# Kernel tuning notes

Hardware: AMD Instinct MI355X
Metric: run time of the kernel (lower is better)

## Reference

```python
import jax, jax.numpy as jnp
import numpy as np

DIM = 180      # channel dim C
HEADS = 6      # num_heads
WS = 8         # window_size
HIDDEN = int(DIM * 4.0)  # mlp hidden = 720
HEAD_DIM = DIM // HEADS  # 30


def layernorm(x, scale, bias, eps=1e-5):
    m = jnp.mean(x, axis=-1, keepdims=True)
    v = jnp.var(x, axis=-1, keepdims=True)
    return (x - m) * jax.lax.rsqrt(v + eps) * scale + bias


def setup_inputs() -> dict:
    key = jax.random.key(0)
    ks = jax.random.split(key, 16)
    B, H, W = 4, 256, 256
    s = 0.02  # weight init scale for numerical sanity
    return {
        "x": jax.random.normal(ks[0], (B, H * W, DIM), jnp.float32),
        "norm1_scale": jnp.ones((DIM,), jnp.float32),
        "norm1_bias": jnp.zeros((DIM,), jnp.float32),
        "qkv_w": jax.random.normal(ks[1], (DIM, 3 * DIM), jnp.float32) * s,  # [in,out] == torch W.T
        "qkv_b": jax.random.normal(ks[2], (3 * DIM,), jnp.float32) * s,
        "proj_w": jax.random.normal(ks[3], (DIM, DIM), jnp.float32) * s,
        "proj_b": jax.random.normal(ks[4], (DIM,), jnp.float32) * s,
        "norm2_scale": jnp.ones((DIM,), jnp.float32),
        "norm2_bias": jnp.zeros((DIM,), jnp.float32),
        "mlp_w1": jax.random.normal(ks[5], (DIM, HIDDEN), jnp.float32) * s,
        "mlp_b1": jax.random.normal(ks[6], (HIDDEN,), jnp.float32) * s,
        "mlp_w2": jax.random.normal(ks[7], (HIDDEN, DIM), jnp.float32) * s,
        "mlp_b2": jax.random.normal(ks[8], (DIM,), jnp.float32) * s,
        "H": H,
        "W": W,
    }


def reference(x, norm1_scale, norm1_bias, qkv_w, qkv_b, proj_w, proj_b,
              norm2_scale, norm2_bias, mlp_w1, mlp_b1, mlp_w2, mlp_b2, H, W):
    B, L, C = x.shape
    shortcut = x
    h = layernorm(x, norm1_scale, norm1_bias).reshape(B, H, W, C)
    # pad to multiples of window size (no-op when H,W % WS == 0)
    pad_b = (WS - H % WS) % WS
    pad_r = (WS - W % WS) % WS
    h = jnp.pad(h, ((0, 0), (0, pad_b), (0, pad_r), (0, 0)))
    Hp, Wp = H + pad_b, W + pad_r
    # window_partition: (B,Hp,Wp,C) -> (nW*B, WS*WS, C)
    win = h.reshape(B, Hp // WS, WS, Wp // WS, WS, C)
    win = win.transpose(0, 1, 3, 2, 4, 5).reshape(-1, WS * WS, C)
    Bw, N, _ = win.shape
    # fused qkv projection
    qkv = (win @ qkv_w + qkv_b).reshape(Bw, N, 3, HEADS, HEAD_DIM)
    qkv = qkv.transpose(2, 0, 3, 1, 4)  # (3, Bw, heads, N, head_dim)
    q, k, v = qkv[0], qkv[1], qkv[2]
    q = q * (HEAD_DIM ** -0.5)
    attn = jax.nn.softmax(jnp.einsum('bhnd,bhmd->bhnm', q, k), axis=-1)
    o = jnp.einsum('bhnm,bhmd->bhnd', attn, v)
    o = o.transpose(0, 2, 1, 3).reshape(Bw, N, C)
    o = o @ proj_w + proj_b
    # window_reverse: (nW*B, WS*WS, C) -> (B,Hp,Wp,C)
    h = o.reshape(B, Hp // WS, Wp // WS, WS, WS, C)
    h = h.transpose(0, 1, 3, 2, 4, 5).reshape(B, Hp, Wp, C)
    h = h[:, :H, :W, :].reshape(B, H * W, C)
    x = shortcut + h
    # MLP with exact (erf) GELU, matching torch nn.GELU default
    y = layernorm(x, norm2_scale, norm2_bias)
    y = jax.nn.gelu(y @ mlp_w1 + mlp_b1, approximate=False) @ mlp_w2 + mlp_b2
    return x + y
```

## Files before the change

kernel.cpp:

```cpp
#include <hip/hip_runtime.h>

typedef unsigned int u32;
typedef unsigned short u16;
typedef __attribute__((ext_vector_type(8))) __bf16 bf16x8;
typedef __attribute__((ext_vector_type(4))) float f32x4;

#define MFMA(a,b,c) __builtin_amdgcn_mfma_f32_16x16x32_bf16(a,b,c,0,0,0)

__device__ __forceinline__ float bf2f(u16 v){ return __uint_as_float(((u32)v) << 16); }
__device__ __forceinline__ u16 f2bf(float f){
  u32 u = __float_as_uint(f);
  u += 0x7fffu + ((u >> 16) & 1u);
  return (u16)(u >> 16);
}
__device__ __forceinline__ u32 pack2(float a, float b){
  return (u32)f2bf(a) | ((u32)f2bf(b) << 16);
}
__device__ __forceinline__ float gelu_fast(float v){
  float t = v*(-1.5957691216f - 0.0713548163f*v*v);
  return v * __builtin_amdgcn_rcpf(1.f + __expf(t));
}

#define QSCALE 0.18257418583505536f

#define OQKV 0
#define OWP  147456
#define OW1  196608
#define OW2  344064
#define NW_TOT 532480

__global__ void swin_unpack(const float* __restrict__ qkvw, const float* __restrict__ projw,
                            const float* __restrict__ w1, const float* __restrict__ w2,
                            u16* __restrict__ ws){
  int idx = blockIdx.x * 256 + threadIdx.x;
  if (idx >= NW_TOT) return;
  float val = 0.f;
  if (idx < OWP){
    int t = idx, nt = t / 3072, r = t % 3072, kt = r >> 9, e = r & 511;
    int lane = e >> 3, j = e & 7;
    int n = nt*16 + (lane & 15), k = kt*32 + (lane >> 4)*8 + j;
    if (n < 576){
      int p = n / 192, c = n - p*192;
      if (c < 180 && k < 180){
        val = qkvw[k*540 + p*180 + c];
        if (p == 0) val *= QSCALE;
      }
    }
  } else if (idx < OW1){
    int t = idx - OWP, nt = t / 3072, r = t % 3072, kt = r >> 9, e = r & 511;
    int lane = e >> 3, j = e & 7;
    int n = nt*16 + (lane & 15), k = kt*32 + (lane >> 4)*8 + j;
    if (n < 180 && k < 180) val = projw[k*180 + n];
  } else if (idx < OW2){
    int t = idx - OW1, nt = t / 3072, r = t % 3072, kt = r >> 9, e = r & 511;
    int lane = e >> 3, j = e & 7;
    int n = nt*16 + (lane & 15), k = kt*32 + (lane >> 4)*8 + j;
    if (n < 720 && k < 180) val = w1[k*720 + n];
  } else {
    int t = idx - OW2, nt = t / 11776, r = t % 11776, kt = r >> 9, e = r & 511;
    int lane = e >> 3, j = e & 7;
    int n = nt*16 + (lane & 15), k = kt*32 + (lane >> 4)*8 + j;
    if (n < 180 && k < 720) val = w2[k*180 + n];
  }
  ws[idx] = f2bf(val);
}

#define A_Y   0
#define A_Q   25600
#define A_K   51200
#define A_VT  76800
#define A_P   104448
#define A_RB  141312

__global__ __launch_bounds__(1024, 1) void swin_attn(
    const float* __restrict__ x, const float* __restrict__ n1s, const float* __restrict__ n1b,
    const u16* __restrict__ ws, const float* __restrict__ qkvb,
    const float* __restrict__ projb, float* __restrict__ out){
  __shared__ __align__(16) char sm[141568];
  const int tid = threadIdx.x;
  const int w16 = tid >> 6, l = tid & 63, l15 = l & 15, lq = l >> 4;
  int* rb = (int*)(sm + A_RB);
  const f32x4 fz = {0.f, 0.f, 0.f, 0.f};
  float4 xv[3];
  const int r4 = l & 3, lq4 = l >> 2;
  const int myrow = w16*4 + r4;

  if (tid < 64){
    int wb = blockIdx.x;
    int b = wb >> 10, wy = (wb >> 5) & 31, wx = wb & 31;
    rb[tid] = b*65536 + (wy*8 + (tid>>3))*256 + (wx*8 + (tid&7));
  }
  for (int i = tid; i < 2304; i += 1024){
    int row = i / 36, t = i - row*36;
    if (t < 24){
      int buf = (t >= 12) ? A_K : A_Q; int tt = t % 12;
      *(u16*)(sm + buf + row*400 + ((tt>>1)*32 + 30 + (tt&1))*2) = 0;
    } else
      *(u16*)(sm + A_Y + row*400 + (180 + t - 24)*2) = 0;
  }
  __syncthreads();

  {
    const float4* px = (const float4*)(x + (size_t)rb[myrow]*180);
    xv[0] = px[lq4];
    xv[1] = px[lq4 + 16];
    xv[2] = (lq4 < 13) ? px[lq4 + 32] : make_float4(0.f,0.f,0.f,0.f);
    float s = 0.f, ss = 0.f;
    #pragma unroll
    for (int i = 0; i < 3; ++i){
      s  += xv[i].x + xv[i].y + xv[i].z + xv[i].w;
      ss += xv[i].x*xv[i].x + xv[i].y*xv[i].y + xv[i].z*xv[i].z + xv[i].w*xv[i].w;
    }
    #pragma unroll
    for (int m = 4; m <= 32; m <<= 1){ s += __shfl_xor(s, m); ss += __shfl_xor(ss, m); }
    float mean = s * (1.f/180.f);
    float rstd = rsqrtf(ss * (1.f/180.f) - mean*mean + 1e-5f);
    u32* yr = (u32*)(sm + A_Y + myrow*400);
    const float4* s4 = (const float4*)n1s;
    const float4* b4 = (const float4*)n1b;
    #pragma unroll
    for (int i = 0; i < 3; ++i){
      if (i < 2 || lq4 < 13){
        int c4 = lq4 + 16*i;
        float4 sc = s4[c4], bi = b4[c4];
        float e0 = (xv[i].x - mean)*rstd*sc.x + bi.x;
        float e1 = (xv[i].y - mean)*rstd*sc.y + bi.y;
        float e2 = (xv[i].z - mean)*rstd*sc.z + bi.z;
        float e3 = (xv[i].w - mean)*rstd*sc.w + bi.w;
        yr[c4*2]     = pack2(e0, e1);
        yr[c4*2 + 1] = pack2(e2, e3);
      }
    }
  }
  __syncthreads();

  {
    const int ntb = w16*3;
    f32x4 acc[4][3];
    #pragma unroll
    for (int m = 0; m < 4; ++m)
      #pragma unroll
      for (int i = 0; i < 3; ++i) acc[m][i] = fz;
    bf16x8 bcur[3];
    #pragma unroll
    for (int i = 0; i < 3; ++i)
      bcur[i] = *(const bf16x8*)(ws + OQKV + ((ntb+i)*6 + 0)*512 + l*8);
    #pragma unroll
    for (int kt = 0; kt < 6; ++kt){
      bf16x8 bnxt[3];
      if (kt < 5){
        #pragma unroll
        for (int i = 0; i < 3; ++i)
          bnxt[i] = *(const bf16x8*)(ws + OQKV + ((ntb+i)*6 + kt + 1)*512 + l*8);
      }
      bf16x8 a[4];
      #pragma unroll
      for (int m = 0; m < 4; ++m)
        a[m] = *(const bf16x8*)(sm + A_Y + (m*16 + l15)*400 + kt*64 + lq*16);
      #pragma unroll
      for (int m = 0; m < 4; ++m)
        #pragma unroll
        for (int i = 0; i < 3; ++i)
          acc[m][i] = MFMA(a[m], bcur[i], acc[m][i]);
      if (kt < 5){
        #pragma unroll
        for (int i = 0; i < 3; ++i) bcur[i] = bnxt[i];
      }
    }
    #pragma unroll
    for (int i = 0; i < 3; ++i){
      int n = (ntb + i)*16 + l15;
      if (n < 576){
        int p = n / 192, c = n - p*192;
        if (c < 180){
          float bias = qkvb[p*180 + c];
          if (p == 0) bias *= QSCALE;
          int h = c / 30, d = c - h*30;
          int colp = h*32 + d;
          #pragma unroll
          for (int m = 0; m < 4; ++m)
            #pragma unroll
            for (int r = 0; r < 4; ++r){
              float val = acc[m][i][r] + bias;
              int tok = m*16 + lq*4 + r;
              if (p == 0)      *(u16*)(sm + A_Q + tok*400 + colp*2) = f2bf(val);
              else if (p == 1) *(u16*)(sm + A_K + tok*400 + colp*2) = f2bf(val);
              else             *(u16*)(sm + A_VT + colp*144 + tok*2) = f2bf(val);
            }
        }
      }
    }
  }
  __syncthreads();

  {
    for (int u = w16; u < 24; u += 16){
      const int tq = u & 3, h = u >> 2;
      bf16x8 aq = *(const bf16x8*)(sm + A_Q + (tq*16 + l15)*400 + h*64 + lq*16);
      f32x4 s[4];
      #pragma unroll
      for (int nt = 0; nt < 4; ++nt){
        bf16x8 bk = *(const bf16x8*)(sm + A_K + (nt*16 + l15)*400 + h*64 + lq*16);
        s[nt] = MFMA(aq, bk, fz);
      }
      float iv4[4];
      #pragma unroll
      for (int r = 0; r < 4; ++r){
        float mx = fmaxf(fmaxf(s[0][r], s[1][r]), fmaxf(s[2][r], s[3][r]));
        mx = fmaxf(mx, __shfl_xor(mx, 1));
        mx = fmaxf(mx, __shfl_xor(mx, 2));
        mx = fmaxf(mx, __shfl_xor(mx, 4));
        mx = fmaxf(mx, __shfl_xor(mx, 8));
        float e0 = __expf(s[0][r]-mx), e1 = __expf(s[1][r]-mx);
        float e2 = __expf(s[2][r]-mx), e3 = __expf(s[3][r]-mx);
        float sum = e0 + e1 + e2 + e3;
        sum += __shfl_xor(sum,1); sum += __shfl_xor(sum,2);
        sum += __shfl_xor(sum,4); sum += __shfl_xor(sum,8);
        iv4[r] = 1.f / sum;
        char* pr = sm + A_P + w16*2304 + (lq*4 + r)*144 + l15*2;
        *(u16*)(pr)      = f2bf(e0);
        *(u16*)(pr + 32) = f2bf(e1);
        *(u16*)(pr + 64) = f2bf(e2);
        *(u16*)(pr + 96) = f2bf(e3);
      }
      asm volatile("s_waitcnt lgkmcnt(0)" ::: "memory");
      f32x4 o0 = fz, o1 = fz;
      #pragma unroll
      for (int kt = 0; kt < 2; ++kt){
        bf16x8 aP  = *(const bf16x8*)(sm + A_P + w16*2304 + l15*144 + kt*64 + lq*16);
        bf16x8 bv0 = *(const bf16x8*)(sm + A_VT + (h*32 + l15)*144 + kt*64 + lq*16);
        bf16x8 bv1 = *(const bf16x8*)(sm + A_VT + (h*32 + 16 + l15)*144 + kt*64 + lq*16);
        o0 = MFMA(aP, bv0, o0);
        o1 = MFMA(aP, bv1, o1);
      }
      #pragma unroll
      for (int r = 0; r < 4; ++r){
        int tok = tq*16 + lq*4 + r;
        {
          int col = h*30 + l15;
          *(u16*)(sm + A_Y + tok*400 + col*2) = f2bf(o0[r] * iv4[r]);
        }
        if (l15 < 14){
          int col = h*30 + 16 + l15;
          *(u16*)(sm + A_Y + tok*400 + col*2) = f2bf(o1[r] * iv4[r]);
        }
      }
    }
  }
  __syncthreads();

  {
    f32x4 acc2[4];
    #pragma unroll
    for (int m = 0; m < 4; ++m) acc2[m] = fz;
    bf16x8 wb0 = *(const bf16x8*)(ws + OWP + (w16*6 + 0)*512 + l*8);
    #pragma unroll
    for (int kt = 0; kt < 6; ++kt){
      bf16x8 wbn;
      if (kt < 5) wbn = *(const bf16x8*)(ws + OWP + (w16*6 + kt + 1)*512 + l*8);
      bf16x8 a[4];
      #pragma unroll
      for (int m = 0; m < 4; ++m)
        a[m] = *(const bf16x8*)(sm + A_Y + (m*16 + l15)*400 + kt*64 + lq*16);
      #pragma unroll
      for (int m = 0; m < 4; ++m)
        acc2[m] = MFMA(a[m], wb0, acc2[m]);
      if (kt < 5) wb0 = wbn;
    }
    float* res = (float*)(sm + A_Q);
    int col = w16*16 + l15;
    if (col < 180){
      float bias = projb[col];
      #pragma unroll
      for (int m = 0; m < 4; ++m)
        #pragma unroll
        for (int r = 0; r < 4; ++r)
          res[(m*16 + lq*4 + r)*180 + col] = acc2[m][r] + bias;
    }
  }
  __syncthreads();

  {
    const float* res = (const float*)(sm + A_Q);
    const float4* rr = (const float4*)(res + myrow*180);
    float4* og = (float4*)(out + (size_t)rb[myrow]*180);
    float4 a0 = rr[lq4];
    a0.x += xv[0].x; a0.y += xv[0].y; a0.z += xv[0].z; a0.w += xv[0].w;
    og[lq4] = a0;
    float4 a1 = rr[lq4 + 16];
    a1.x += xv[1].x; a1.y += xv[1].y; a1.z += xv[1].z; a1.w += xv[1].w;
    og[lq4 + 16] = a1;
    if (lq4 < 13){
      float4 a2 = rr[lq4 + 32];
      a2.x += xv[2].x; a2.y += xv[2].y; a2.z += xv[2].z; a2.w += xv[2].w;
      og[lq4 + 32] = a2;
    }
  }
}

#define M_Y 0
#define M_G 25600

__global__ __launch_bounds__(1024, 1) void swin_mlp(
    const float* __restrict__ n2s, const float* __restrict__ n2b,
    const u16* __restrict__ ws, const float* __restrict__ b1, const float* __restrict__ b2,
    float* __restrict__ out){
  __shared__ __align__(16) char sm[124928];
  const int tid = threadIdx.x;
  const int w16 = tid >> 6, l = tid & 63, l15 = l & 15, lq = l >> 4;
  const size_t base = (size_t)blockIdx.x * (64*180);
  const f32x4 fz = {0.f, 0.f, 0.f, 0.f};
  float4 xv[3];
  const int r4 = l & 3, lq4 = l >> 2;
  const int myrow = w16*4 + r4;

  if (tid < 768){
    int row = tid / 12, col = 180 + tid % 12;
    *(u16*)(sm + M_Y + row*400 + col*2) = 0;
  }
  {
    const float4* px = (const float4*)(out + base + (size_t)myrow*180);
    xv[0] = px[lq4];
    xv[1] = px[lq4 + 16];
    xv[2] = (lq4 < 13) ? px[lq4 + 32] : make_float4(0.f,0.f,0.f,0.f);
    float s = 0.f, ss = 0.f;
    #pragma unroll
    for (int i = 0; i < 3; ++i){
      s  += xv[i].x + xv[i].y + xv[i].z + xv[i].w;
      ss += xv[i].x*xv[i].x + xv[i].y*xv[i].y + xv[i].z*xv[i].z + xv[i].w*xv[i].w;
    }
    #pragma unroll
    for (int m = 4; m <= 32; m <<= 1){ s += __shfl_xor(s, m); ss += __shfl_xor(ss, m); }
    float mean = s * (1.f/180.f);
    float rstd = rsqrtf(ss * (1.f/180.f) - mean*mean + 1e-5f);
    u32* yr = (u32*)(sm + M_Y + myrow*400);
    const float4* s4 = (const float4*)n2s;
    const float4* b4 = (const float4*)n2b;
    #pragma unroll
    for (int i = 0; i < 3; ++i){
      if (i < 2 || lq4 < 13){
        int c4 = lq4 + 16*i;
        float4 sc = s4[c4], bi = b4[c4];
        float e0 = (xv[i].x - mean)*rstd*sc.x + bi.x;
        float e1 = (xv[i].y - mean)*rstd*sc.y + bi.y;
        float e2 = (xv[i].z - mean)*rstd*sc.z + bi.z;
        float e3 = (xv[i].w - mean)*rstd*sc.w + bi.w;
        yr[c4*2]     = pack2(e0, e1);
        yr[c4*2 + 1] = pack2(e2, e3);
      }
    }
  }
  __syncthreads();

  {
    const int ntb = w16*3;
    f32x4 acc[4][3];
    #pragma unroll
    for (int m = 0; m < 4; ++m)
      #pragma unroll
      for (int i = 0; i < 3; ++i) acc[m][i] = fz;
    bf16x8 bcur[3];
    #pragma unroll
    for (int i = 0; i < 3; ++i)
      bcur[i] = *(const bf16x8*)(ws + OW1 + ((ntb+i)*6 + 0)*512 + l*8);
    #pragma unroll
    for (int kt = 0; kt < 6; ++kt){
      bf16x8 bnxt[3];
      if (kt < 5){
        #pragma unroll
        for (int i = 0; i < 3; ++i)
          bnxt[i] = *(const bf16x8*)(ws + OW1 + ((ntb+i)*6 + kt + 1)*512 + l*8);
      }
      bf16x8 a[4];
      #pragma unroll
      for (int m = 0; m < 4; ++m)
        a[m] = *(const bf16x8*)(sm + M_Y + (m*16 + l15)*400 + kt*64 + lq*16);
      #pragma unroll
      for (int m = 0; m < 4; ++m)
        #pragma unroll
        for (int i = 0; i < 3; ++i)
          acc[m][i] = MFMA(a[m], bcur[i], acc[m][i]);
      if (kt < 5){
        #pragma unroll
        for (int i = 0; i < 3; ++i) bcur[i] = bnxt[i];
      }
    }
    #pragma unroll
    for (int i = 0; i < 3; ++i){
      int gc = (ntb + i)*16 + l15;
      float bias = (gc < 720) ? b1[gc] : 0.f;
      #pragma unroll
      for (int m = 0; m < 4; ++m)
        #pragma unroll
        for (int r = 0; r < 4; ++r){
          float v = acc[m][i][r] + bias;
          float gel = (gc < 720) ? gelu_fast(v) : 0.f;
          *(u16*)(sm + M_G + (m*16 + lq*4 + r)*1552 + gc*2) = f2bf(gel);
        }
    }
  }
  __syncthreads();

  {
    f32x4 acc2[4];
    #pragma unroll
    for (int m = 0; m < 4; ++m) acc2[m] = fz;
    bf16x8 wb0, wb1;
    wb0 = *(const bf16x8*)(ws + OW2 + (w16*23 + 0)*512 + l*8);
    wb1 = *(const bf16x8*)(ws + OW2 + (w16*23 + 1)*512 + l*8);
    for (int kt = 0; kt < 23; ++kt){
      int ktn = (kt < 21) ? kt + 2 : 22;
      bf16x8 wbn = *(const bf16x8*)(ws + OW2 + (w16*23 + ktn)*512 + l*8);
      bf16x8 a[4];
      #pragma unroll
      for (int m = 0; m < 4; ++m)
        a[m] = *(const bf16x8*)(sm + M_G + (m*16 + l15)*1552 + kt*64 + lq*16);
      #pragma unroll
      for (int m = 0; m < 4; ++m)
        acc2[m] = MFMA(a[m], wb0, acc2[m]);
      wb0 = wb1; wb1 = wbn;
    }
    __syncthreads();

    float* res = (float*)(sm + M_G);
    int col = w16*16 + l15;
    if (col < 180){
      float bias = b2[col];
      #pragma unroll
      for (int m = 0; m < 4; ++m)
        #pragma unroll
        for (int r = 0; r < 4; ++r)
          res[(m*16 + lq*4 + r)*180 + col] = acc2[m][r] + bias;
    }
  }
  __syncthreads();

  {
    const float* res = (const float*)(sm + M_G);
    const float4* rr = (const float4*)(res + myrow*180);
    float4* og = (float4*)(out + base + (size_t)myrow*180);
    float4 a0 = rr[lq4];
    a0.x += xv[0].x; a0.y += xv[0].y; a0.z += xv[0].z; a0.w += xv[0].w;
    og[lq4] = a0;
    float4 a1 = rr[lq4 + 16];
    a1.x += xv[1].x; a1.y += xv[1].y; a1.z += xv[1].z; a1.w += xv[1].w;
    og[lq4 + 16] = a1;
    if (lq4 < 13){
      float4 a2 = rr[lq4 + 32];
      a2.x += xv[2].x; a2.y += xv[2].y; a2.z += xv[2].z; a2.w += xv[2].w;
      og[lq4 + 32] = a2;
    }
  }
}

extern "C" void kernel_launch(void* const* d_in, const int* in_sizes, int n_in,
                              void* d_out, int out_size, void* d_ws, size_t ws_size,
                              hipStream_t stream){
  const float* x     = (const float*)d_in[0];
  const float* n1s   = (const float*)d_in[1];
  const float* n1b   = (const float*)d_in[2];
  const float* qkvw  = (const float*)d_in[3];
  const float* qkvb  = (const float*)d_in[4];
  const float* projw = (const float*)d_in[5];
  const float* projb = (const float*)d_in[6];
  const float* n2s   = (const float*)d_in[7];
  const float* n2b   = (const float*)d_in[8];
  const float* w1    = (const float*)d_in[9];
  const float* b1    = (const float*)d_in[10];
  const float* w2    = (const float*)d_in[11];
  const float* b2    = (const float*)d_in[12];
  float* outp = (float*)d_out;
  u16* wsp = (u16*)d_ws;

  swin_unpack<<<(NW_TOT + 255) / 256, 256, 0, stream>>>(qkvw, projw, w1, w2, wsp);
  swin_attn<<<4096, 1024, 0, stream>>>(x, n1s, n1b, wsp, qkvb, projb, outp);
  swin_mlp<<<4096, 1024, 0, stream>>>(n2s, n2b, wsp, b1, b2, outp);
}
```

Measured before the change: 566.3 us.

## Shrink attention block to 12 waves and drop shared row-index table

```diff
diff --git a/kernel.cpp b/kernel.cpp
--- a/kernel.cpp
+++ b/kernel.cpp
@@ -70,27 +70,23 @@
 #define A_K   51200
 #define A_VT  76800
 #define A_P   104448
-#define A_RB  141312
-
-__global__ __launch_bounds__(1024, 1) void swin_attn(
+
+__global__ __launch_bounds__(768, 1) void swin_attn(
     const float* __restrict__ x, const float* __restrict__ n1s, const float* __restrict__ n1b,
     const u16* __restrict__ ws, const float* __restrict__ qkvb,
     const float* __restrict__ projb, float* __restrict__ out){
-  __shared__ __align__(16) char sm[141568];
+  __shared__ __align__(16) char sm[132096];
   const int tid = threadIdx.x;
-  const int w16 = tid >> 6, l = tid & 63, l15 = l & 15, lq = l >> 4;
-  int* rb = (int*)(sm + A_RB);
+  const int w12 = tid >> 6, l = tid & 63, l15 = l & 15, lq = l >> 4;
   const f32x4 fz = {0.f, 0.f, 0.f, 0.f};
-  float4 xv[3];
-  const int r4 = l & 3, lq4 = l >> 2;
-  const int myrow = w16*4 + r4;
-
-  if (tid < 64){
-    int wb = blockIdx.x;
-    int b = wb >> 10, wy = (wb >> 5) & 31, wx = wb & 31;
-    rb[tid] = b*65536 + (wy*8 + (tid>>3))*256 + (wx*8 + (tid&7));
-  }
-  for (int i = tid; i < 2304; i += 1024){
+  const int wb = blockIdx.x;
+  const int bb = wb >> 10, wy = (wb >> 5) & 31, wx = wb & 31;
+  const int r3 = l & 7, lq2 = l >> 3;
+  const int myrow = w12*8 + r3;
+  const size_t myglob = (size_t)(bb*65536 + (wy*8 + (myrow >> 3))*256 + wx*8 + (myrow & 7)) * 180;
+  float4 xv[6];
+
+  for (int i = tid; i < 2304; i += 768){
     int row = i / 36, t = i - row*36;
     if (t < 24){
       int buf = (t >= 12) ? A_K : A_Q; int tt = t % 12;
@@ -98,30 +94,29 @@
     } else
       *(u16*)(sm + A_Y + row*400 + (180 + t - 24)*2) = 0;
   }
-  __syncthreads();
-
-  {
-    const float4* px = (const float4*)(x + (size_t)rb[myrow]*180);
-    xv[0] = px[lq4];
-    xv[1] = px[lq4 + 16];
-    xv[2] = (lq4 < 13) ? px[lq4 + 32] : make_float4(0.f,0.f,0.f,0.f);
+
+  if (w12 < 8){
+    const float4* px = (const float4*)(x + myglob);
+    #pragma unroll
+    for (int i = 0; i < 5; ++i) xv[i] = px[lq2 + 8*i];
+    xv[5] = (lq2 < 5) ? px[lq2 + 40] : make_float4(0.f,0.f,0.f,0.f);
     float s = 0.f, ss = 0.f;
     #pragma unroll
-    for (int i = 0; i < 3; ++i){
+    for (int i = 0; i < 6; ++i){
       s  += xv[i].x + xv[i].y + xv[i].z + xv[i].w;
       ss += xv[i].x*xv[i].x + xv[i].y*xv[i].y + xv[i].z*xv[i].z + xv[i].w*xv[i].w;
     }
     #pragma unroll
-    for (int m = 4; m <= 32; m <<= 1){ s += __shfl_xor(s, m); ss += __shfl_xor(ss, m); }
+    for (int m = 8; m <= 32; m <<= 1){ s += __shfl_xor(s, m); ss += __shfl_xor(ss, m); }
     float mean = s * (1.f/180.f);
     float rstd = rsqrtf(ss * (1.f/180.f) - mean*mean + 1e-5f);
     u32* yr = (u32*)(sm + A_Y + myrow*400);
     const float4* s4 = (const float4*)n1s;
     const float4* b4 = (const float4*)n1b;
     #pragma unroll
-    for (int i = 0; i < 3; ++i){
-      if (i < 2 || lq4 < 13){
-        int c4 = lq4 + 16*i;
+    for (int i = 0; i < 6; ++i){
+      if (i < 5 || lq2 < 5){
+        int c4 = lq2 + 8*i;
         float4 sc = s4[c4], bi = b4[c4];
         float e0 = (xv[i].x - mean)*rstd*sc.x + bi.x;
         float e1 = (xv[i].y - mean)*rstd*sc.y + bi.y;
@@ -135,7 +130,7 @@
   __syncthreads();
 
   {
-    const int ntb = w16*3;
+    const int ntb = w12*3;
     f32x4 acc[4][3];
     #pragma unroll
     for (int m = 0; m < 4; ++m)
@@ -170,31 +165,29 @@
     #pragma unroll
     for (int i = 0; i < 3; ++i){
       int n = (ntb + i)*16 + l15;
-      if (n < 576){
-        int p = n / 192, c = n - p*192;
-        if (c < 180){
-          float bias = qkvb[p*180 + c];
-          if (p == 0) bias *= QSCALE;
-          int h = c / 30, d = c - h*30;
-          int colp = h*32 + d;
+      int p = n / 192, c = n - p*192;
+      if (c < 180){
+        float bias = qkvb[p*180 + c];
+        if (p == 0) bias *= QSCALE;
+        int h = c / 30, d = c - h*30;
+        int colp = h*32 + d;
+        #pragma unroll
+        for (int m = 0; m < 4; ++m)
           #pragma unroll
-          for (int m = 0; m < 4; ++m)
-            #pragma unroll
-            for (int r = 0; r < 4; ++r){
-              float val = acc[m][i][r] + bias;
-              int tok = m*16 + lq*4 + r;
-              if (p == 0)      *(u16*)(sm + A_Q + tok*400 + colp*2) = f2bf(val);
-              else if (p == 1) *(u16*)(sm + A_K + tok*400 + colp*2) = f2bf(val);
-              else             *(u16*)(sm + A_VT + colp*144 + tok*2) = f2bf(val);
-            }
-        }
-      }
-    }
-  }
-  __syncthreads();
-
-  {
-    for (int u = w16; u < 24; u += 16){
+          for (int r = 0; r < 4; ++r){
+            float val = acc[m][i][r] + bias;
+            int tok = m*16 + lq*4 + r;
+            if (p == 0)      *(u16*)(sm + A_Q + tok*400 + colp*2) = f2bf(val);
+            else if (p == 1) *(u16*)(sm + A_K + tok*400 + colp*2) = f2bf(val);
+            else             *(u16*)(sm + A_VT + colp*144 + tok*2) = f2bf(val);
+          }
+      }
+    }
+  }
+  __syncthreads();
+
+  {
+    for (int u = w12; u < 24; u += 12){
       const int tq = u & 3, h = u >> 2;
       bf16x8 aq = *(const bf16x8*)(sm + A_Q + (tq*16 + l15)*400 + h*64 + lq*16);
       f32x4 s[4];
@@ -217,7 +210,7 @@
         sum += __shfl_xor(sum,1); sum += __shfl_xor(sum,2);
         sum += __shfl_xor(sum,4); sum += __shfl_xor(sum,8);
         iv4[r] = 1.f / sum;
-        char* pr = sm + A_P + w16*2304 + (lq*4 + r)*144 + l15*2;
+        char* pr = sm + A_P + w12*2304 + (lq*4 + r)*144 + l15*2;
         *(u16*)(pr)      = f2bf(e0);
         *(u16*)(pr + 32) = f2bf(e1);
         *(u16*)(pr + 64) = f2bf(e2);
@@ -227,7 +220,7 @@
       f32x4 o0 = fz, o1 = fz;
       #pragma unroll
       for (int kt = 0; kt < 2; ++kt){
-        bf16x8 aP  = *(const bf16x8*)(sm + A_P + w16*2304 + l15*144 + kt*64 + lq*16);
+        bf16x8 aP  = *(const bf16x8*)(sm + A_P + w12*2304 + l15*144 + kt*64 + lq*16);
         bf16x8 bv0 = *(const bf16x8*)(sm + A_VT + (h*32 + l15)*144 + kt*64 + lq*16);
         bf16x8 bv1 = *(const bf16x8*)(sm + A_VT + (h*32 + 16 + l15)*144 + kt*64 + lq*16);
         o0 = MFMA(aP, bv0, o0);
@@ -253,11 +246,11 @@
     f32x4 acc2[4];
     #pragma unroll
     for (int m = 0; m < 4; ++m) acc2[m] = fz;
-    bf16x8 wb0 = *(const bf16x8*)(ws + OWP + (w16*6 + 0)*512 + l*8);
+    bf16x8 wb0 = *(const bf16x8*)(ws + OWP + (w12*6 + 0)*512 + l*8);
     #pragma unroll
     for (int kt = 0; kt < 6; ++kt){
       bf16x8 wbn;
-      if (kt < 5) wbn = *(const bf16x8*)(ws + OWP + (w16*6 + kt + 1)*512 + l*8);
+      if (kt < 5) wbn = *(const bf16x8*)(ws + OWP + (w12*6 + kt + 1)*512 + l*8);
       bf16x8 a[4];
       #pragma unroll
       for (int m = 0; m < 4; ++m)
@@ -268,7 +261,7 @@
       if (kt < 5) wb0 = wbn;
     }
     float* res = (float*)(sm + A_Q);
-    int col = w16*16 + l15;
+    int col = w12*16 + l15;
     if (col < 180){
       float bias = projb[col];
       #pragma unroll
@@ -280,20 +273,18 @@
   }
   __syncthreads();
 
-  {
+  if (w12 < 8){
     const float* res = (const float*)(sm + A_Q);
     const float4* rr = (const float4*)(res + myrow*180);
-    float4* og = (float4*)(out + (size_t)rb[myrow]*180);
-    float4 a0 = rr[lq4];
-    a0.x += xv[0].x; a0.y += xv[0].y; a0.z += xv[0].z; a0.w += xv[0].w;
-    og[lq4] = a0;
-    float4 a1 = rr[lq4 + 16];
-    a1.x += xv[1].x; a1.y += xv[1].y; a1.z += xv[1].z; a1.w += xv[1].w;
-    og[lq4 + 16] = a1;
-    if (lq4 < 13){
-      float4 a2 = rr[lq4 + 32];
-      a2.x += xv[2].x; a2.y += xv[2].y; a2.z += xv[2].z; a2.w += xv[2].w;
-      og[lq4 + 32] = a2;
+    float4* og = (float4*)(out + myglob);
+    #pragma unroll
+    for (int i = 0; i < 6; ++i){
+      if (i < 5 || lq2 < 5){
+        int c4 = lq2 + 8*i;
+        float4 a = rr[c4];
+        a.x += xv[i].x; a.y += xv[i].y; a.z += xv[i].z; a.w += xv[i].w;
+        og[c4] = a;
+      }
     }
   }
 }
@@ -473,6 +464,6 @@
   u16* wsp = (u16*)d_ws;
 
   swin_unpack<<<(NW_TOT + 255) / 256, 256, 0, stream>>>(qkvw, projw, w1, w2, wsp);
-  swin_attn<<<4096, 1024, 0, stream>>>(x, n1s, n1b, wsp, qkvb, projb, outp);
+  swin_attn<<<4096, 768, 0, stream>>>(x, n1s, n1b, wsp, qkvb, projb, outp);
   swin_mlp<<<4096, 1024, 0, stream>>>(n2s, n2b, wsp, b1, b2, outp);
 }
```

New measurement: 564.2 us. No clear change (-0.4%).
